# Performance work log

Measured on AMD Instinct MI355X. Metric: run time of the kernel, lower is better.

## Reference

```python
import jax, jax.numpy as jnp
import numpy as np

DIM, DEPTH, HEADS = 1024, 6, 16
B, N = 2, 1024
QB = 128.0   # 8-bit activation absmax quant: Qb = 2**(8-1)
EPS = 1e-5


def setup_inputs() -> dict:
    key = jax.random.key(0)
    ks = jax.random.split(key, 4)
    x = jax.random.normal(ks[0], (B, N, DIM), dtype=jnp.float32)
    # BitLinear weights (per layer, two per FFN block), latent fp weights
    ff_w1 = jax.random.normal(ks[1], (DEPTH, DIM, DIM), dtype=jnp.float32) * 0.02
    ff_w2 = jax.random.normal(ks[2], (DEPTH, DIM, DIM), dtype=jnp.float32) * 0.02
    # LayerNorm params (inside FeedForward) and final norm
    ff_ln_g = jnp.ones((DEPTH, DIM), jnp.float32)
    ff_ln_b = jnp.zeros((DEPTH, DIM), jnp.float32)
    final_ln_g = jnp.ones((DIM,), jnp.float32)
    final_ln_b = jnp.zeros((DIM,), jnp.float32)
    return dict(x=x, ff_ln_g=ff_ln_g, ff_ln_b=ff_ln_b, ff_w1=ff_w1,
                ff_w2=ff_w2, final_ln_g=final_ln_g, final_ln_b=final_ln_b)


def layernorm(x, g, b):
    m = jnp.mean(x, axis=-1, keepdims=True)
    v = jnp.mean((x - m) ** 2, axis=-1, keepdims=True)
    return (x - m) * jax.lax.rsqrt(v + EPS) * g + b


def bitlinear(x, w):
    # BitNet b1: binarize weights around their mean, absmax-quantize activations to 8 bits,
    # int-style matmul, then rescale by beta*gamma/Qb.
    alpha = jnp.mean(w)
    w_b = jnp.sign(w - alpha)                 # ternary/binary weights {-1,0,+1}
    beta = jnp.mean(jnp.abs(w))               # ||W||_1 / (n*m)
    gamma = jnp.max(jnp.abs(x))               # activation absmax
    x_q = jnp.clip(x * (QB / gamma), -QB + EPS, QB - EPS)
    y = jnp.einsum('...i,oi->...o', x_q, w_b)
    return y * (beta * gamma / QB)


def attend(x):
    # non-flash multi-head self-attention, q=k=v=x (Attend has no projections)
    b, n, d = x.shape
    dh = d // HEADS
    q = x.reshape(b, n, HEADS, dh).transpose(0, 2, 1, 3)          # bhnd
    scores = jnp.einsum('bhid,bhjd->bhij', q, q) * (dh ** -0.5)   # [B,H,N,N]
    attn = jax.nn.softmax(scores, axis=-1)
    out = jnp.einsum('bhij,bhjd->bhid', attn, q)
    return out.transpose(0, 2, 1, 3).reshape(b, n, d)


def reference(x, ff_ln_g, ff_ln_b, ff_w1, ff_w2, final_ln_g, final_ln_b):
    for i in range(DEPTH):
        x = attend(x) + x
        h = layernorm(x, ff_ln_g[i], ff_ln_b[i])
        h = bitlinear(h, ff_w1[i])
        h = jax.nn.gelu(h, approximate=False)   # torch nn.GELU default = exact
        h = bitlinear(h, ff_w2[i])
        x = h + x
    return layernorm(x, final_ln_g, final_ln_b)
```

## Files before the change

### kernel.cpp

```cpp
#include <hip/hip_runtime.h>
#include <math.h>

typedef __attribute__((ext_vector_type(4))) float f32x4;
typedef __attribute__((ext_vector_type(8))) _Float16 f16x8;

__device__ __forceinline__ f32x4 mfma16h(f16x8 a, f16x8 b, f32x4 c){
  return __builtin_amdgcn_mfma_f32_16x16x32_f16(a, b, c, 0, 0, 0);
}
__device__ __forceinline__ void gload_lds16(const void* g, void* l){
  __builtin_amdgcn_global_load_lds((const __attribute__((address_space(1))) void*)g,
                                   (__attribute__((address_space(3))) void*)l, 16, 0, 0);
}

#define EXPC 0.1803368801111204f
#define PHI(n) (((((n)>>3)&1)<<2) | ((((n)>>1)&1)<<1) | ((n)&1))

__global__ __launch_bounds__(256) void k_wstats(const float* __restrict__ w1, const float* __restrict__ w2,
                                                double* __restrict__ dsum, double* __restrict__ dabs){
  const int mat = blockIdx.y;
  const float* wp = (mat < 6) ? (w1 + (size_t)mat*1048576) : (w2 + (size_t)(mat-6)*1048576);
  const f32x4* wv = (const f32x4*)wp + (size_t)blockIdx.x*8192;
  double s = 0.0, a = 0.0;
  for (int j = 0; j < 32; j++){
    f32x4 v = wv[j*256 + threadIdx.x];
    s += (double)v.x + (double)v.y + (double)v.z + (double)v.w;
    a += (double)fabsf(v.x) + (double)fabsf(v.y) + (double)fabsf(v.z) + (double)fabsf(v.w);
  }
  for (int d = 1; d < 64; d <<= 1){ s += __shfl_xor(s, d); a += __shfl_xor(a, d); }
  __shared__ double red[8];
  const int w = threadIdx.x >> 6;
  if ((threadIdx.x & 63) == 0){ red[w*2] = s; red[w*2+1] = a; }
  __syncthreads();
  if (threadIdx.x == 0){
    double S = red[0]+red[2]+red[4]+red[6], A = red[1]+red[3]+red[5]+red[7];
    atomicAdd(&dsum[mat], S);
    atomicAdd(&dabs[mat], A);
  }
}

__global__ __launch_bounds__(256) void k_binarize(const float* __restrict__ w1, const float* __restrict__ w2,
                                                  const double* __restrict__ dsum, _Float16* __restrict__ wb){
  const int blk = blockIdx.x;
  const int mat = blk >> 9;
  const float alpha = (float)(dsum[mat] * (1.0/1048576.0));
  const float* wp = (mat < 6) ? (w1 + (size_t)mat*1048576) : (w2 + (size_t)(mat-6)*1048576);
  const size_t off = (size_t)(blk & 511)*2048 + (size_t)threadIdx.x*8;
  const int n = (int)(off >> 10), k = (int)(off & 1023);
  f32x4 v0 = *(const f32x4*)(wp + off), v1 = *(const f32x4*)(wp + off + 4);
  float vv[8] = {v0.x,v0.y,v0.z,v0.w,v1.x,v1.y,v1.z,v1.w};
  f16x8 pk;
  #pragma unroll
  for (int e = 0; e < 8; e++){
    float d = vv[e] - alpha;
    pk[e] = d > 0.f ? (_Float16)1.0f : (d < 0.f ? (_Float16)(-1.0f) : (_Float16)0.0f);
  }
  const size_t addr = (size_t)mat*1048576 + (size_t)n*1024 + (size_t)((k & ~63) + ((k & 63) ^ ((n&7)*8)));
  *(f16x8*)&wb[addr] = pk;
}

__global__ __launch_bounds__(256) void k_presplit(const float* __restrict__ x,
                                                  _Float16* __restrict__ Kh, _Float16* __restrict__ Kl,
                                                  _Float16* __restrict__ Vh, _Float16* __restrict__ Vl){
  __shared__ _Float16 lh[64*72], ll[64*72];
  const int t = blockIdx.x, bh = blockIdx.y, b = bh>>4, h = bh&15;
  const int n = threadIdx.x>>2, c0 = (threadIdx.x&3)*16;
  const float* src = x + (size_t)b*1048576 + (size_t)(t*64+n)*1024 + h*64 + c0;
  const size_t kbase = ((size_t)bh*1024 + t*64 + n)*64;
  const int sw = PHI(n)*8;
  #pragma unroll
  for (int j = 0; j < 2; j++){
    f32x4 v0 = *(const f32x4*)(src + j*8);
    f32x4 v1 = *(const f32x4*)(src + j*8 + 4);
    float vv[8] = {v0.x,v0.y,v0.z,v0.w,v1.x,v1.y,v1.z,v1.w};
    f16x8 Hv, Lv;
    #pragma unroll
    for (int e = 0; e < 8; e++){
      _Float16 hh = (_Float16)vv[e];
      Hv[e] = hh; Lv[e] = (_Float16)(vv[e] - (float)hh);
      const int d = c0 + j*8 + e;
      lh[d*72 + n] = Hv[e]; ll[d*72 + n] = Lv[e];
    }
    const int db = c0 + j*8;
    *(f16x8*)&Kh[kbase + (db ^ sw)] = Hv;
    *(f16x8*)&Kl[kbase + (db ^ sw)] = Lv;
  }
  __syncthreads();
  const int d = threadIdx.x>>2, n0c = (threadIdx.x&3)*16;
  const size_t vbase = ((size_t)bh*64 + d)*1024 + t*64;
  const int sw2 = (d&7)*8;
  #pragma unroll
  for (int j = 0; j < 2; j++){
    const int nb = n0c + j*8;
    *(f16x8*)&Vh[vbase + (nb ^ sw2)] = *(const f16x8*)&lh[d*72 + nb];
    *(f16x8*)&Vl[vbase + (nb ^ sw2)] = *(const f16x8*)&ll[d*72 + nb];
  }
}

__global__ __launch_bounds__(256) void k_attn(const _Float16* __restrict__ Kh, const _Float16* __restrict__ Kl,
                                              const _Float16* __restrict__ Vh, const _Float16* __restrict__ Vl,
                                              const float* __restrict__ xin, float* __restrict__ xout){
  __shared__ _Float16 smb[40960];
  const int tid = threadIdx.x, w = tid>>6, l = tid&63, g = l>>4, r16 = l&15;
  const int bh = blockIdx.x, qt = blockIdx.y, b = bh>>4, h = bh&15;
  const _Float16* Kbh = Kh + (size_t)bh*65536;
  const _Float16* Kbl = Kl + (size_t)bh*65536;

  size_t koffK[2], voff[2];
  int cbj[2];
  #pragma unroll
  for (int j = 0; j < 2; j++){
    const int cb = (j*4 + w)*64, c = cb + l;
    const int p  = c>>3;
    const int kp = (p&32) | ((p&12)<<1) | ((p&16)>>2) | (p&3);
    cbj[j]   = cb;
    koffK[j] = (size_t)kp*64 + (size_t)(l&7)*8;
    voff[j]  = ((size_t)bh*64 + (c>>3))*1024 + (size_t)(c&7)*8;
  }
  #define KSTAGE(PK, T) { _Pragma("unroll")                                          \
    for (int j = 0; j < 2; j++){                                                      \
      gload_lds16(Kbh + (size_t)(T)*4096 + koffK[j], (PK) + cbj[j]*8);                \
      gload_lds16(Kbl + (size_t)(T)*4096 + koffK[j], (PK) + 4096 + cbj[j]*8);         \
    } }
  #define VSTAGE(PV, T) { _Pragma("unroll")                                          \
    for (int j = 0; j < 2; j++){                                                      \
      gload_lds16(Vh + voff[j] + (T)*64, (PV) + cbj[j]*8);                            \
      gload_lds16(Vl + voff[j] + (T)*64, (PV) + 4096 + cbj[j]*8);                     \
    } }

  _Float16* pKo = smb;
  _Float16* pKn = smb + 8192;
  _Float16* pKs = smb + 16384;
  _Float16* pVc = smb + 24576;
  _Float16* pVs = smb + 32768;

  KSTAGE(pKo, 0); KSTAGE(pKn, 1); VSTAGE(pVc, 0);
  const int qrow = w*16 + r16;
  const int phq8 = PHI(qrow)*8;
  const size_t qb = (size_t)qt*4096 + (size_t)qrow*64;
  const f16x8 aqh0 = *(const f16x8*)&Kbh[qb + ((g*8) ^ phq8)];
  const f16x8 aqh1 = *(const f16x8*)&Kbh[qb + ((32 + g*8) ^ phq8)];
  const f16x8 aql0 = *(const f16x8*)&Kbl[qb + ((g*8) ^ phq8)];
  const f16x8 aql1 = *(const f16x8*)&Kbl[qb + ((32 + g*8) ^ phq8)];
  __syncthreads();

  const int swk8 = (r16&7)*8;
  float mI = -1e30f, lI = 0.f;
  f32x4 acc[4], sA[4], sB[4];
  #pragma unroll
  for (int i = 0; i < 4; i++) acc[i] = (f32x4){0.f,0.f,0.f,0.f};

  #define QKT(PK, SD) { const _Float16* kt_h = (PK); const _Float16* kt_l = (PK) + 4096;  \
    _Pragma("unroll")                                                                      \
    for (int c = 0; c < 4; c++){                                                           \
      const int rk = c*16 + r16;                                                           \
      const f16x8 kh0 = *(const f16x8*)&kt_h[rk*64 + ((g*8) ^ swk8)];                      \
      const f16x8 kh1 = *(const f16x8*)&kt_h[rk*64 + ((32+g*8) ^ swk8)];                   \
      const f16x8 kl0 = *(const f16x8*)&kt_l[rk*64 + ((g*8) ^ swk8)];                      \
      const f16x8 kl1 = *(const f16x8*)&kt_l[rk*64 + ((32+g*8) ^ swk8)];                   \
      f32x4 z = (f32x4){0.f,0.f,0.f,0.f};                                                  \
      z = mfma16h(kh0, aqh0, z);                                                           \
      z = mfma16h(kh1, aqh1, z);                                                           \
      z = mfma16h(kh0, aql0, z);                                                           \
      z = mfma16h(kh1, aql1, z);                                                           \
      z = mfma16h(kl0, aqh0, z);                                                           \
      z = mfma16h(kl1, aqh1, z);                                                           \
      (SD)[c] = z;                                                                         \
    } }

  #define SMAXPV(SC) {                                                                     \
    float rmax = (SC)[0][0];                                                               \
    _Pragma("unroll")                                                                      \
    for (int c = 0; c < 4; c++)                                                            \
      _Pragma("unroll")                                                                    \
      for (int i = 0; i < 4; i++) rmax = fmaxf(rmax, (SC)[c][i]);                          \
    rmax = fmaxf(rmax, __shfl_xor(rmax, 16));                                              \
    rmax = fmaxf(rmax, __shfl_xor(rmax, 32));                                              \
    if (__any(rmax - mI > 44.36f)){                                                        \
      const float mn = fmaxf(mI, rmax);                                                    \
      const float fac = exp2f((mI - mn)*EXPC);                                             \
      lI *= fac;                                                                           \
      mI = mn;                                                                             \
      _Pragma("unroll")                                                                    \
      for (int i = 0; i < 4; i++){                                                         \
        const float fi = __shfl(fac, g*4 + i);                                             \
        _Pragma("unroll")                                                                  \
        for (int dc = 0; dc < 4; dc++) acc[dc][i] *= fi;                                   \
      }                                                                                    \
    }                                                                                      \
    const float mC = mI*EXPC;                                                              \
    float rsum = 0.f;                                                                      \
    f16x8 aph[2], apl[2];                                                                  \
    _Pragma("unroll")                                                                      \
    for (int c = 0; c < 4; c++)                                                            \
      _Pragma("unroll")                                                                    \
      for (int i = 0; i < 4; i++){                                                         \
        const float p = exp2f(fmaf((SC)[c][i], EXPC, -mC));                                \
        const _Float16 ph = (_Float16)p;                                                   \
        aph[c>>1][(c&1)*4 + i] = ph;                                                       \
        apl[c>>1][(c&1)*4 + i] = (_Float16)(p - (float)ph);                                \
        rsum += p;                                                                         \
      }                                                                                    \
    rsum += __shfl_xor(rsum, 16);                                                          \
    rsum += __shfl_xor(rsum, 32);                                                          \
    lI += rsum;                                                                            \
    const _Float16* vt_h = pVc; const _Float16* vt_l = pVc + 4096;                         \
    _Pragma("unroll")                                                                      \
    for (int ks = 0; ks < 2; ks++){                                                        \
      _Pragma("unroll")                                                                    \
      for (int dc = 0; dc < 4; dc++){                                                      \
        const int vr = dc*16 + r16;                                                        \
        const f16x8 bvh = *(const f16x8*)&vt_h[vr*64 + ((ks*32 + g*8) ^ swk8)];            \
        const f16x8 bvl = *(const f16x8*)&vt_l[vr*64 + ((ks*32 + g*8) ^ swk8)];            \
        acc[dc] = mfma16h(aph[ks], bvh, acc[dc]);                                          \
        acc[dc] = mfma16h(apl[ks], bvh, acc[dc]);                                          \
        acc[dc] = mfma16h(aph[ks], bvl, acc[dc]);                                          \
      }                                                                                    \
    } }

  QKT(pKo, sA);

  for (int tt = 0; tt < 8; tt++){
    {
      const int t = 2*tt;
      if (t < 14) KSTAGE(pKs, t+2);
      VSTAGE(pVs, t+1);
      QKT(pKn, sB);
      SMAXPV(sA);
      __syncthreads();
      _Float16* tk = pKo; pKo = pKn; pKn = pKs; pKs = tk;
      _Float16* tv = pVc; pVc = pVs; pVs = tv;
    }
    {
      const int t = 2*tt+1;
      if (t < 14) KSTAGE(pKs, t+2);
      if (t < 15) VSTAGE(pVs, t+1);
      if (t < 15) QKT(pKn, sA);
      SMAXPV(sB);
      __syncthreads();
      _Float16* tk = pKo; pKo = pKn; pKn = pKs; pKs = tk;
      _Float16* tv = pVc; pVc = pVs; pVs = tv;
    }
  }
  #undef KSTAGE
  #undef VSTAGE
  #undef QKT
  #undef SMAXPV

  #pragma unroll
  for (int i = 0; i < 4; i++){
    const float li = __shfl(lI, g*4 + i);
    const float inv = 1.f/li;
    const int row = qt*64 + w*16 + g*4 + i;
    #pragma unroll
    for (int dc = 0; dc < 4; dc++){
      const size_t idx = (size_t)b*1048576 + (size_t)row*1024 + h*64 + dc*16 + r16;
      xout[idx] = acc[dc][i]*inv + xin[idx];
    }
  }
}

template<int SPLIT>
__global__ __launch_bounds__(256) void k_ln(const float* __restrict__ x, const float* __restrict__ gg,
                                            const float* __restrict__ bb, float* __restrict__ outf,
                                            _Float16* __restrict__ Oh, _Float16* __restrict__ Ol){
  const int row = blockIdx.x*4 + (threadIdx.x>>6);
  const int lane = threadIdx.x & 63;
  const float* xr = x + (size_t)row*1024;
  f32x4 v[4];
  float s = 0.f, q = 0.f;
  #pragma unroll
  for (int c = 0; c < 2; c++){
    v[c*2]   = *(const f32x4*)(xr + c*512 + lane*8);
    v[c*2+1] = *(const f32x4*)(xr + c*512 + lane*8 + 4);
    #pragma unroll
    for (int e = 0; e < 4; e++){
      s += v[c*2][e] + v[c*2+1][e];
      q += v[c*2][e]*v[c*2][e] + v[c*2+1][e]*v[c*2+1][e];
    }
  }
  for (int d = 1; d < 64; d <<= 1){ s += __shfl_xor(s,d); q += __shfl_xor(q,d); }
  const float mean = s * (1.f/1024.f);
  const float var  = q * (1.f/1024.f) - mean*mean;
  const float rstd = rsqrtf(var + 1e-5f);
  #pragma unroll
  for (int c = 0; c < 2; c++){
    const int col = c*512 + lane*8;
    f32x4 g0 = *(const f32x4*)(gg + col), g1 = *(const f32x4*)(gg + col + 4);
    f32x4 b0 = *(const f32x4*)(bb + col), b1 = *(const f32x4*)(bb + col + 4);
    float h[8];
    #pragma unroll
    for (int e = 0; e < 4; e++){
      h[e]   = (v[c*2][e]  -mean)*rstd*g0[e] + b0[e];
      h[e+4] = (v[c*2+1][e]-mean)*rstd*g1[e] + b1[e];
    }
    if (SPLIT){
      f16x8 Hv, Lv;
      #pragma unroll
      for (int e = 0; e < 8; e++){
        _Float16 hh = (_Float16)h[e];
        Hv[e] = hh; Lv[e] = (_Float16)(h[e] - (float)hh);
      }
      const size_t addr = (size_t)row*1024 + c*512 + (lane>>3)*64 + (((lane&7)*8) ^ ((row&7)*8));
      *(f16x8*)&Oh[addr] = Hv;
      *(f16x8*)&Ol[addr] = Lv;
    } else {
      f32x4 o0, o1;
      #pragma unroll
      for (int e = 0; e < 4; e++){ o0[e] = h[e]; o1[e] = h[e+4]; }
      *(f32x4*)(outf + (size_t)row*1024 + col) = o0;
      *(f32x4*)(outf + (size_t)row*1024 + col + 4) = o1;
    }
  }
}

template<int MODE>
__global__ __launch_bounds__(256) void k_gemm(const _Float16* __restrict__ Ah, const _Float16* __restrict__ Al,
                                              const _Float16* __restrict__ Wg,
                                              float* __restrict__ out32,
                                              _Float16* __restrict__ Oh, _Float16* __restrict__ Ol,
                                              const double* __restrict__ dabs_slot,
                                              _Float16* __restrict__ Kh, _Float16* __restrict__ Kl,
                                              _Float16* __restrict__ Vh, _Float16* __restrict__ Vl){
  __shared__ _Float16 smb[24576];
  const int tid = threadIdx.x, w = tid>>6, l = tid&63, g = l>>4, r16 = l&15;
  const int wm = w>>1, wn = w&1;
  const int n0 = blockIdx.x*64, m0 = blockIdx.y*64;
  const float scale = (float)(*dabs_slot * (1.0/1048576.0));
  const int swr = (r16&7)*8;
  f32x4 acc[2][2] = {};
  #define STAGE(buf, k0) { _Float16* Bp = smb + (buf)*12288;                              \
    _Pragma("unroll")                                                                     \
    for (int j = 0; j < 2; j++){                                                          \
      const int cb = (j*4 + w)*64; const int c = cb + l;                                  \
      const int r = c>>3; const int cc = (c&7)*8;                                         \
      gload_lds16(Ah + (size_t)(m0 + r)*1024 + (k0) + cc, Bp + cb*8);                     \
      gload_lds16(Al + (size_t)(m0 + r)*1024 + (k0) + cc, Bp + 4096 + cb*8);              \
      gload_lds16(Wg + (size_t)(n0 + r)*1024 + (k0) + cc, Bp + 8192 + cb*8);              \
    } }
  STAGE(0, 0);
  __syncthreads();
  for (int t = 0; t < 16; t++){
    if (t < 15) STAGE((t+1)&1, (t+1)*64);
    const _Float16* Bp = smb + (t&1)*12288;
    #pragma unroll
    for (int kk = 0; kk < 2; kk++){
      f16x8 ah[2], al[2], bf[2];
      const int col = (kk*32 + g*8) ^ swr;
      #pragma unroll
      for (int mi = 0; mi < 2; mi++){
        const int row = wm*32 + mi*16 + r16;
        ah[mi] = *(const f16x8*)&Bp[row*64 + col];
        al[mi] = *(const f16x8*)&Bp[4096 + row*64 + col];
      }
      #pragma unroll
      for (int ni = 0; ni < 2; ni++){
        const int row = wn*32 + ni*16 + r16;
        bf[ni] = *(const f16x8*)&Bp[8192 + row*64 + col];
      }
      #pragma unroll
      for (int mi = 0; mi < 2; mi++)
        #pragma unroll
        for (int ni = 0; ni < 2; ni++){
          acc[mi][ni] = mfma16h(ah[mi], bf[ni], acc[mi][ni]);
          acc[mi][ni] = mfma16h(al[mi], bf[ni], acc[mi][ni]);
        }
    }
    __syncthreads();
  }
  #undef STAGE
  _Float16* kh_t = smb;
  _Float16* kl_t = smb + 4608;
  _Float16* lhv  = smb + 9216;
  _Float16* llv  = smb + 13824;
  #pragma unroll
  for (int mi = 0; mi < 2; mi++)
    #pragma unroll
    for (int ni = 0; ni < 2; ni++)
      #pragma unroll
      for (int i = 0; i < 4; i++){
        const int rr = m0 + wm*32 + mi*16 + g*4 + i;
        const int cc = n0 + wn*32 + ni*16 + r16;
        float vv = acc[mi][ni][i] * scale;
        if (MODE == 0){
          vv = 0.5f*vv*(1.f + erff(vv*0.70710678118f));
          _Float16 hh = (_Float16)vv;
          const size_t addr = (size_t)rr*1024 + (cc & ~63) + ((cc & 63) ^ ((rr&7)*8));
          Oh[addr] = hh;
          Ol[addr] = (_Float16)(vv - (float)hh);
        } else {
          const size_t idx = (size_t)rr*1024 + cc;
          const float xnew = out32[idx] + vv;
          out32[idx] = xnew;
          if (Kh){
            const int nl = wm*32 + mi*16 + g*4 + i;
            const int dl = wn*32 + ni*16 + r16;
            const _Float16 hh = (_Float16)xnew;
            const _Float16 lo = (_Float16)(xnew - (float)hh);
            kh_t[nl*72 + dl] = hh;  kl_t[nl*72 + dl] = lo;
            lhv [dl*72 + nl] = hh;  llv [dl*72 + nl] = lo;
          }
        }
      }
  if (MODE == 1 && Kh){
    __syncthreads();
    const int n = tid>>2, c0q = (tid&3)*16;
    const int bh = (blockIdx.y>>4)*16 + blockIdx.x;
    const int tseq = blockIdx.y & 15;
    const size_t kbase = ((size_t)bh*1024 + tseq*64 + n)*64;
    const int swn = PHI(n)*8;
    const size_t vbase = ((size_t)bh*64 + n)*1024 + tseq*64;
    const int sw2 = (n&7)*8;
    #pragma unroll
    for (int j = 0; j < 2; j++){
      const int db = c0q + j*8;
      *(f16x8*)&Kh[kbase + (db ^ swn)] = *(const f16x8*)&kh_t[n*72 + db];
      *(f16x8*)&Kl[kbase + (db ^ swn)] = *(const f16x8*)&kl_t[n*72 + db];
      *(f16x8*)&Vh[vbase + (db ^ sw2)] = *(const f16x8*)&lhv[n*72 + db];
      *(f16x8*)&Vl[vbase + (db ^ sw2)] = *(const f16x8*)&llv[n*72 + db];
    }
  }
}

extern "C" void kernel_launch(void* const* d_in, const int* in_sizes, int n_in,
                              void* d_out, int out_size, void* d_ws, size_t ws_size,
                              hipStream_t stream){
  const float* x_in = (const float*)d_in[0];
  const float* ln_g = (const float*)d_in[1];
  const float* ln_b = (const float*)d_in[2];
  const float* w1   = (const float*)d_in[3];
  const float* w2   = (const float*)d_in[4];
  const float* fg   = (const float*)d_in[5];
  const float* fb   = (const float*)d_in[6];

  char* ws = (char*)d_ws;
  double*   dsum  = (double*)ws;
  double*   dabs  = (double*)(ws + 96);
  _Float16* wb = (_Float16*)(ws + 256);
  size_t o = 256 + 12ull*1048576ull*2ull;
  float* xA = (float*)(ws + o); o += 2048ull*1024*4;
  float* xB = (float*)(ws + o); o += 2048ull*1024*4;
  _Float16* Kh = (_Float16*)(ws + o); o += 2048ull*1024*2;
  _Float16* Kl = (_Float16*)(ws + o); o += 2048ull*1024*2;
  _Float16* Vh = (_Float16*)(ws + o); o += 2048ull*1024*2;
  _Float16* Vl = (_Float16*)(ws + o); o += 2048ull*1024*2;
  _Float16* Ahb = (_Float16*)(ws + o); o += 2048ull*1024*2;
  _Float16* Alb = (_Float16*)(ws + o); o += 2048ull*1024*2;
  _Float16* Ghb = (_Float16*)(ws + o); o += 2048ull*1024*2;
  _Float16* Glb = (_Float16*)(ws + o); o += 2048ull*1024*2;

  hipMemsetAsync(ws, 0, 256, stream);
  k_wstats  <<<dim3(32,12), 256, 0, stream>>>(w1, w2, dsum, dabs);
  k_binarize<<<6144,        256, 0, stream>>>(w1, w2, dsum, wb);
  k_presplit<<<dim3(16,32), 256, 0, stream>>>(x_in, Kh, Kl, Vh, Vl);

  const float* xc = x_in;
  for (int i = 0; i < 6; i++){
    float* xn = (i & 1) ? xB : xA;
    const bool last = (i == 5);
    k_attn    <<<dim3(32,16), 256, 0, stream>>>(Kh, Kl, Vh, Vl, xc, xn);
    k_ln<1>   <<<512, 256, 0, stream>>>(xn, ln_g + (size_t)i*1024, ln_b + (size_t)i*1024,
                                        nullptr, Ahb, Alb);
    k_gemm<0> <<<dim3(16,32), 256, 0, stream>>>(Ahb, Alb, wb + (size_t)i*1048576,
                                                nullptr, Ghb, Glb, &dabs[i],
                                                nullptr, nullptr, nullptr, nullptr);
    k_gemm<1> <<<dim3(16,32), 256, 0, stream>>>(Ghb, Glb, wb + (size_t)(6+i)*1048576,
                                                xn, nullptr, nullptr, &dabs[6+i],
                                                last ? nullptr : Kh, last ? nullptr : Kl,
                                                last ? nullptr : Vh, last ? nullptr : Vl);
    xc = xn;
  }
  k_ln<0><<<512, 256, 0, stream>>>(xc, fg, fb, (float*)d_out, nullptr, nullptr);
}
```

Before: 509.5 us.

## Pre-pack binarized weights in MFMA fragment order and load B directly to registers

The binarize kernel now writes weights in a blocked layout that matches the MFMA B-fragment order (16 rows by 32 k per 512-element chunk). The GEMM loads its B operands straight from global memory into registers with register double-buffering, so the LDS staging for weights goes away. This cuts LDS traffic and footprint, which may allow higher occupancy. The cost is more register pressure, plus global loads that are not shared across the wm warps, so each weight tile is fetched twice per block.

New measurement: 528.4 us. +3.7%, slower.

```diff
diff --git a/kernel.cpp b/kernel.cpp
--- a/kernel.cpp
+++ b/kernel.cpp
@@ -54,7 +54,8 @@
     float d = vv[e] - alpha;
     pk[e] = d > 0.f ? (_Float16)1.0f : (d < 0.f ? (_Float16)(-1.0f) : (_Float16)0.0f);
   }
-  const size_t addr = (size_t)mat*1048576 + (size_t)n*1024 + (size_t)((k & ~63) + ((k & 63) ^ ((n&7)*8)));
+  const size_t addr = (size_t)mat*1048576 +
+      ((((size_t)(n>>4)*32 + (k>>5))*64) + (size_t)((k>>3)&3)*16 + (n&15))*8;
   *(f16x8*)&wb[addr] = pk;
 }
 
@@ -321,30 +322,41 @@
                                               const double* __restrict__ dabs_slot,
                                               _Float16* __restrict__ Kh, _Float16* __restrict__ Kl,
                                               _Float16* __restrict__ Vh, _Float16* __restrict__ Vl){
-  __shared__ _Float16 smb[24576];
+  __shared__ _Float16 smb[18432];
   const int tid = threadIdx.x, w = tid>>6, l = tid&63, g = l>>4, r16 = l&15;
   const int wm = w>>1, wn = w&1;
   const int n0 = blockIdx.x*64, m0 = blockIdx.y*64;
+  const int nc0 = blockIdx.x*4;
   const float scale = (float)(*dabs_slot * (1.0/1048576.0));
   const int swr = (r16&7)*8;
   f32x4 acc[2][2] = {};
-  #define STAGE(buf, k0) { _Float16* Bp = smb + (buf)*12288;                              \
+  #define STAGE(buf, k0) { _Float16* Bp = smb + (buf)*8192;                               \
     _Pragma("unroll")                                                                     \
     for (int j = 0; j < 2; j++){                                                          \
       const int cb = (j*4 + w)*64; const int c = cb + l;                                  \
       const int r = c>>3; const int cc = (c&7)*8;                                         \
       gload_lds16(Ah + (size_t)(m0 + r)*1024 + (k0) + cc, Bp + cb*8);                     \
       gload_lds16(Al + (size_t)(m0 + r)*1024 + (k0) + cc, Bp + 4096 + cb*8);              \
-      gload_lds16(Wg + (size_t)(n0 + r)*1024 + (k0) + cc, Bp + 8192 + cb*8);              \
     } }
+  #define BLOAD(T, B00, B01, B10, B11) {                                                  \
+    const size_t ksb = (size_t)(T)*2;                                                     \
+    (B00) = *(const f16x8*)&Wg[(((size_t)(nc0 + wn*2 + 0))*32 + ksb+0)*512 + (size_t)l*8];\
+    (B01) = *(const f16x8*)&Wg[(((size_t)(nc0 + wn*2 + 1))*32 + ksb+0)*512 + (size_t)l*8];\
+    (B10) = *(const f16x8*)&Wg[(((size_t)(nc0 + wn*2 + 0))*32 + ksb+1)*512 + (size_t)l*8];\
+    (B11) = *(const f16x8*)&Wg[(((size_t)(nc0 + wn*2 + 1))*32 + ksb+1)*512 + (size_t)l*8];}
+  f16x8 bc00, bc01, bc10, bc11, bn00, bn01, bn10, bn11;
+  BLOAD(0, bc00, bc01, bc10, bc11);
   STAGE(0, 0);
   __syncthreads();
   for (int t = 0; t < 16; t++){
-    if (t < 15) STAGE((t+1)&1, (t+1)*64);
-    const _Float16* Bp = smb + (t&1)*12288;
+    if (t < 15){
+      STAGE((t+1)&1, (t+1)*64);
+      BLOAD(t+1, bn00, bn01, bn10, bn11);
+    }
+    const _Float16* Bp = smb + (t&1)*8192;
     #pragma unroll
     for (int kk = 0; kk < 2; kk++){
-      f16x8 ah[2], al[2], bf[2];
+      f16x8 ah[2], al[2];
       const int col = (kk*32 + g*8) ^ swr;
       #pragma unroll
       for (int mi = 0; mi < 2; mi++){
@@ -352,22 +364,21 @@
         ah[mi] = *(const f16x8*)&Bp[row*64 + col];
         al[mi] = *(const f16x8*)&Bp[4096 + row*64 + col];
       }
+      const f16x8 bf0 = kk ? bc10 : bc00;
+      const f16x8 bf1 = kk ? bc11 : bc01;
       #pragma unroll
-      for (int ni = 0; ni < 2; ni++){
-        const int row = wn*32 + ni*16 + r16;
-        bf[ni] = *(const f16x8*)&Bp[8192 + row*64 + col];
+      for (int mi = 0; mi < 2; mi++){
+        acc[mi][0] = mfma16h(ah[mi], bf0, acc[mi][0]);
+        acc[mi][0] = mfma16h(al[mi], bf0, acc[mi][0]);
+        acc[mi][1] = mfma16h(ah[mi], bf1, acc[mi][1]);
+        acc[mi][1] = mfma16h(al[mi], bf1, acc[mi][1]);
       }
-      #pragma unroll
-      for (int mi = 0; mi < 2; mi++)
-        #pragma unroll
-        for (int ni = 0; ni < 2; ni++){
-          acc[mi][ni] = mfma16h(ah[mi], bf[ni], acc[mi][ni]);
-          acc[mi][ni] = mfma16h(al[mi], bf[ni], acc[mi][ni]);
-        }
     }
     __syncthreads();
+    bc00 = bn00; bc01 = bn01; bc10 = bn10; bc11 = bn11;
   }
   #undef STAGE
+  #undef BLOAD
   _Float16* kh_t = smb;
   _Float16* kl_t = smb + 4608;
   _Float16* lhv  = smb + 9216;
```
